# Kernel tuning notes

Measured on AMD Instinct MI355X. Metric: run time of the kernel, lower is better.

Reference implementation:

```python
import jax, jax.numpy as jnp
import numpy as np

B, S, D, H, L, V, P = 4, 1024, 768, 12, 12, 50257, 1024
HD = D // H  # 64
EPS = 1e-5


def setup_inputs() -> dict:
    key = jax.random.key(0)
    ks = jax.random.split(key, 9)
    s = 0.02
    n = lambda k, shape: (jax.random.normal(k, shape, jnp.float32) * s)
    return {
        "input_ids": jax.random.randint(ks[0], (B, S), 0, V),
        "wte": n(ks[1], (V, D)),
        "wpe": n(ks[2], (P, D)),
        "ln1_w": jnp.ones((L, D), jnp.float32),
        "ln1_b": jnp.zeros((L, D), jnp.float32),
        "attn_w": n(ks[3], (L, D, 3 * D)),
        "attn_b": jnp.zeros((L, 3 * D), jnp.float32),
        "atp_w": n(ks[4], (L, D, D)),
        "atp_b": jnp.zeros((L, D), jnp.float32),
        "ln2_w": jnp.ones((L, D), jnp.float32),
        "ln2_b": jnp.zeros((L, D), jnp.float32),
        "fc_w": n(ks[5], (L, D, 4 * D)),
        "fc_b": jnp.zeros((L, 4 * D), jnp.float32),
        "pj_w": n(ks[6], (L, 4 * D, D)),
        "pj_b": jnp.zeros((L, D), jnp.float32),
        "lnf_w": jnp.ones((D,), jnp.float32),
        "lnf_b": jnp.zeros((D,), jnp.float32),
        "lm_w": n(ks[7], (D, V)),
    }


def _ln(x, w, b):
    m = x.mean(-1, keepdims=True)
    v = ((x - m) ** 2).mean(-1, keepdims=True)
    return (x - m) * jax.lax.rsqrt(v + EPS) * w + b


def reference(input_ids, wte, wpe, ln1_w, ln1_b, attn_w, attn_b, atp_w, atp_b,
              ln2_w, ln2_b, fc_w, fc_b, pj_w, pj_b, lnf_w, lnf_b, lm_w):
    h = wte[input_ids] + wpe[jnp.arange(S)][None]  # [B,S,D]
    scale = 1.0 / jnp.sqrt(jnp.float32(HD))
    for l in range(L):
        # attention block (no causal mask in original)
        x = _ln(h, ln1_w[l], ln1_b[l])
        qkv = x @ attn_w[l] + attn_b[l]
        q, k, v = jnp.split(qkv, 3, axis=-1)
        q = q.reshape(B, S, H, HD)
        k = k.reshape(B, S, H, HD)
        v = v.reshape(B, S, H, HD)
        att = jnp.einsum('bqhd,bkhd->bhqk', q, k) * scale
        att = jax.nn.softmax(att, axis=-1)
        y = jnp.einsum('bhqk,bkhd->bqhd', att, v).reshape(B, S, D)
        h = h + y @ atp_w[l] + atp_b[l]
        # MLP block (exact erf GELU, torch nn.GELU default)
        x = _ln(h, ln2_w[l], ln2_b[l])
        h = h + jax.nn.gelu(x @ fc_w[l] + fc_b[l], approximate=False) @ pj_w[l] + pj_b[l]
    h = _ln(h, lnf_w, lnf_b)
    return h @ lm_w  # [B,S,V] logits
```

## Files before the change

### kernel.cpp

```cpp
#include <hip/hip_runtime.h>
#include <hip/hip_bf16.h>
#include <cstdint>

#define DEVI __device__ __forceinline__

typedef __attribute__((ext_vector_type(8))) short bf16x8_t;
typedef __attribute__((ext_vector_type(4))) float f32x4_t;

DEVI float bf2f(unsigned short u) {
    union { uint32_t i; float f; } v; v.i = ((uint32_t)u) << 16; return v.f;
}
DEVI unsigned short f2bf(float f) {
    union { float f; uint32_t i; } v; v.f = f;
    uint32_t i = v.i;
    uint32_t r = (i + 0x7FFFu + ((i >> 16) & 1u)) >> 16;
    return (unsigned short)r;
}

DEVI f32x4_t mfma16(bf16x8_t a, bf16x8_t b, f32x4_t c) {
    return __builtin_amdgcn_mfma_f32_16x16x32_bf16(a, b, c, 0, 0, 0);
}

#define GL2LDS(g, l) __builtin_amdgcn_global_load_lds( \
    (const __attribute__((address_space(1))) void*)(g), \
    (__attribute__((address_space(3))) void*)(l), 16, 0, 0)

__global__ void k_embed_ln(const int* __restrict__ ids, const float* __restrict__ wte,
                           const float* __restrict__ wpe, const float* __restrict__ w,
                           const float* __restrict__ b, float* __restrict__ h,
                           unsigned short* __restrict__ x) {
    int m = blockIdx.x;
    int s = m & 1023;
    int id = ids[m];
    int t = threadIdx.x;
    const float4 te = *reinterpret_cast<const float4*>(wte + (size_t)id * 768 + t * 4);
    const float4 pe = *reinterpret_cast<const float4*>(wpe + (size_t)s * 768 + t * 4);
    float4 v; v.x = te.x + pe.x; v.y = te.y + pe.y; v.z = te.z + pe.z; v.w = te.w + pe.w;
    *reinterpret_cast<float4*>(h + (size_t)m * 768 + t * 4) = v;
    float sm = v.x + v.y + v.z + v.w;
    float ss = v.x * v.x + v.y * v.y + v.z * v.z + v.w * v.w;
#pragma unroll
    for (int o = 32; o > 0; o >>= 1) { sm += __shfl_down(sm, o); ss += __shfl_down(ss, o); }
    __shared__ float red[8];
    int wid = t >> 6, lane = t & 63;
    if (lane == 0) { red[wid] = sm; red[4 + wid] = ss; }
    __syncthreads();
    if (t == 0) {
        float S = red[0] + red[1] + red[2];
        float SS = red[4] + red[5] + red[6];
        float mean = S * (1.f / 768.f);
        float var = SS * (1.f / 768.f) - mean * mean;
        red[0] = mean; red[1] = rsqrtf(var + 1e-5f);
    }
    __syncthreads();
    float mean = red[0], rst = red[1];
    float4 wv = *reinterpret_cast<const float4*>(w + t * 4);
    float4 bv = *reinterpret_cast<const float4*>(b + t * 4);
    ushort4 o4;
    o4.x = f2bf((v.x - mean) * rst * wv.x + bv.x);
    o4.y = f2bf((v.y - mean) * rst * wv.y + bv.y);
    o4.z = f2bf((v.z - mean) * rst * wv.z + bv.z);
    o4.w = f2bf((v.w - mean) * rst * wv.w + bv.w);
    *reinterpret_cast<ushort4*>(x + (size_t)m * 768 + t * 4) = o4;
}

__global__ void k_ln_red(const unsigned short* __restrict__ part, const float* __restrict__ ab,
                         const float* __restrict__ w, const float* __restrict__ b,
                         float* __restrict__ h, unsigned short* __restrict__ x) {
    int m = blockIdx.x;
    int t = threadIdx.x;
    size_t o0 = (size_t)m * 768 + t * 4;
    float4 hv = *reinterpret_cast<const float4*>(h + o0);
    ushort4 q0 = *reinterpret_cast<const ushort4*>(part + o0);
    ushort4 q1 = *reinterpret_cast<const ushort4*>(part + 4096ull * 768 + o0);
    float4 av = *reinterpret_cast<const float4*>(ab + t * 4);
    float4 v;
    v.x = hv.x + bf2f(q0.x) + bf2f(q1.x) + av.x;
    v.y = hv.y + bf2f(q0.y) + bf2f(q1.y) + av.y;
    v.z = hv.z + bf2f(q0.z) + bf2f(q1.z) + av.z;
    v.w = hv.w + bf2f(q0.w) + bf2f(q1.w) + av.w;
    float sm = v.x + v.y + v.z + v.w;
    float ss = v.x * v.x + v.y * v.y + v.z * v.z + v.w * v.w;
#pragma unroll
    for (int o = 32; o > 0; o >>= 1) { sm += __shfl_down(sm, o); ss += __shfl_down(ss, o); }
    __shared__ float red[8];
    int wid = t >> 6, lane = t & 63;
    if (lane == 0) { red[wid] = sm; red[4 + wid] = ss; }
    __syncthreads();
    if (t == 0) {
        float S = red[0] + red[1] + red[2];
        float SS = red[4] + red[5] + red[6];
        float mean = S * (1.f / 768.f);
        float var = SS * (1.f / 768.f) - mean * mean;
        red[0] = mean; red[1] = rsqrtf(var + 1e-5f);
    }
    __syncthreads();
    float mean = red[0], rst = red[1];
    *reinterpret_cast<float4*>(h + o0) = v;
    float4 wv = *reinterpret_cast<const float4*>(w + t * 4);
    float4 bv = *reinterpret_cast<const float4*>(b + t * 4);
    ushort4 o4;
    o4.x = f2bf((v.x - mean) * rst * wv.x + bv.x);
    o4.y = f2bf((v.y - mean) * rst * wv.y + bv.y);
    o4.z = f2bf((v.z - mean) * rst * wv.z + bv.z);
    o4.w = f2bf((v.w - mean) * rst * wv.w + bv.w);
    *reinterpret_cast<ushort4*>(x + (size_t)m * 768 + t * 4) = o4;
}

__global__ void k_transpose(const float* __restrict__ W, unsigned short* __restrict__ Bt,
                            int K, int N, int Npad) {
    __shared__ float tile[64][65];
    int tx = threadIdx.x, ty = threadIdx.y;
    int n0 = blockIdx.x * 64, k0 = blockIdx.y * 64;
    size_t l = blockIdx.z;
    W += l * (size_t)K * N;
    Bt += l * (size_t)Npad * K;
    if (n0 + 64 <= N) {
#pragma unroll
        for (int i = 0; i < 4; i++) {
            int kr = ty * 4 + i;
            float4 v = *reinterpret_cast<const float4*>(W + (size_t)(k0 + kr) * N + n0 + tx * 4);
            tile[kr][tx * 4 + 0] = v.x;
            tile[kr][tx * 4 + 1] = v.y;
            tile[kr][tx * 4 + 2] = v.z;
            tile[kr][tx * 4 + 3] = v.w;
        }
    } else {
#pragma unroll
        for (int i = 0; i < 4; i++) {
            int kr = ty * 4 + i;
#pragma unroll
            for (int j = 0; j < 4; j++) {
                int n = n0 + tx * 4 + j;
                tile[kr][tx * 4 + j] = (n < N) ? W[(size_t)(k0 + kr) * N + n] : 0.f;
            }
        }
    }
    __syncthreads();
#pragma unroll
    for (int i = 0; i < 4; i++) {
        int n = n0 + ty * 4 + i;
        ushort4 o;
        o.x = f2bf(tile[tx * 4 + 0][ty * 4 + i]);
        o.y = f2bf(tile[tx * 4 + 1][ty * 4 + i]);
        o.z = f2bf(tile[tx * 4 + 2][ty * 4 + i]);
        o.w = f2bf(tile[tx * 4 + 3][ty * 4 + i]);
        *reinterpret_cast<ushort4*>(Bt + (size_t)n * K + k0 + tx * 4) = o;
    }
}

template <int BM, int BIAS, int GELU, int OUTBF16, int SPLITK>
__launch_bounds__(256, 2)
__global__ void k_gemm(const unsigned short* __restrict__ A,
                       const unsigned short* __restrict__ Bt,
                       const float* __restrict__ bias,
                       void* __restrict__ out,
                       int M, int N, int K) {
    constexpr int MF = BM / 32;
    constexpr int HALF = (BM + 128) * 64;
    __shared__ char smem_raw[2 * HALF];

    int t = threadIdx.x;
    int bm = blockIdx.x, bn = blockIdx.y;
    int kc = (SPLITK > 1) ? blockIdx.z : 0;
    int KC = K / SPLITK;

    int rowA0 = bm * BM, rowB0 = bn * 128;
    int lane = t & 63, w = t >> 6;
    int wr = w >> 1, wc = w & 1;

    const unsigned short* ga0 = A  + (size_t)(rowA0 + (t >> 2)) * K + kc * KC + (t & 3) * 8;
    const unsigned short* ga1 = ga0 + (size_t)64 * K;
    const unsigned short* gb0 = Bt + (size_t)(rowB0 + (t >> 2)) * K + kc * KC + (t & 3) * 8;
    const unsigned short* gb1 = gb0 + (size_t)64 * K;

    auto stage = [&](int buf, int ktile) {
        char* dst = smem_raw + buf * HALF + t * 16;
        int kt = ktile * 32;
        GL2LDS(ga0 + kt, dst);
        if constexpr (BM == 128) GL2LDS(ga1 + kt, dst + 4096);
        char* dstB = dst + BM * 64;
        GL2LDS(gb0 + kt, dstB);
        GL2LDS(gb1 + kt, dstB + 4096);
    };

    f32x4_t acc[MF][4] = {};

    int rA = wr * (BM / 2) + (lane & 15);
    int rB = wc * 64 + (lane & 15);
    int kofs = (lane >> 4) * 8;

    const int NT = KC / 32;
    stage(0, 0);
    __syncthreads();
    int cur = 0;
    for (int kt = 0; kt < NT; kt++) {
        if (kt + 1 < NT) stage(cur ^ 1, kt + 1);
        const unsigned short* As = (const unsigned short*)(smem_raw + cur * HALF);
        const unsigned short* Bs = As + BM * 32;
        bf16x8_t a[MF], b[4];
#pragma unroll
        for (int m = 0; m < MF; m++)
            a[m] = *reinterpret_cast<const bf16x8_t*>(As + (rA + m * 16) * 32 + kofs);
#pragma unroll
        for (int n = 0; n < 4; n++)
            b[n] = *reinterpret_cast<const bf16x8_t*>(Bs + (rB + n * 16) * 32 + kofs);
#pragma unroll
        for (int m = 0; m < MF; m++)
#pragma unroll
            for (int n = 0; n < 4; n++)
                acc[m][n] = mfma16(a[m], b[n], acc[m][n]);
        __syncthreads();
        cur ^= 1;
    }

    if constexpr (OUTBF16) {
        int colBase = bn * 128 + wc * 64 + (lane & 15);
        int rowBase = bm * BM + wr * (BM / 2) + ((lane >> 4) << 2);
#pragma unroll
        for (int n = 0; n < 4; n++) {
            int col = colBase + n * 16;
            float bv = 0.f;
            if (BIAS) bv = bias[col];
#pragma unroll
            for (int m = 0; m < MF; m++) {
                int row0 = rowBase + m * 16;
#pragma unroll
                for (int r = 0; r < 4; r++) {
                    int row = row0 + r;
                    float v = acc[m][n][r] + bv;
                    if (GELU) v = 0.5f * v * (1.f + erff(v * 0.70710678118f));
                    ((unsigned short*)out)[(size_t)row * N + col] = f2bf(v);
                }
            }
        }
    } else {
        auto epi = (unsigned short (*)[16][72])smem_raw;
        unsigned short* op_base = (unsigned short*)out + (size_t)kc * M * N;
        int rowBase0 = bm * BM + wr * (BM / 2);
        int colBase0 = bn * 128 + wc * 64;
#pragma unroll
        for (int m = 0; m < MF; m++) {
#pragma unroll
            for (int n = 0; n < 4; n++)
#pragma unroll
                for (int r = 0; r < 4; r++)
                    epi[w][(lane >> 4) * 4 + r][n * 16 + (lane & 15)] = f2bf(acc[m][n][r]);
            __syncthreads();
#pragma unroll
            for (int rr = 0; rr < 4; rr++) {
                int lr = (lane >> 4) * 4 + rr;
                int grow = rowBase0 + m * 16 + lr;
                int gcol = colBase0 + (lane & 15) * 4;
                ushort4 v4 = *reinterpret_cast<ushort4*>(&epi[w][lr][(lane & 15) * 4]);
                *reinterpret_cast<ushort4*>(op_base + (size_t)grow * N + gcol) = v4;
            }
            __syncthreads();
        }
    }
}

__launch_bounds__(512, 1)
__global__ void k_lm(const unsigned short* __restrict__ A,
                     const unsigned short* __restrict__ Bt,
                     float* __restrict__ out) {
    constexpr int K = 768;
    constexpr int NT = K / 64;
    __shared__ char smem[131072];

    int t = threadIdx.x;
    int bm = blockIdx.x, bn = blockIdx.y;
    int lane = t & 63, w = t >> 6;
    int wm = w >> 2, wn = w & 3;
    int q = lane >> 4, l15 = lane & 15, l7 = lane & 7;

    int srow = t >> 3;
    int sslot = (t & 7) ^ (srow & 7);
    const unsigned short* gA = A  + (size_t)(bm * 256 + srow) * K + sslot * 8;
    const unsigned short* gB = Bt + (size_t)(bn * 256 + srow) * K + sslot * 8;

    auto stage = [&](int buf, int ktile) {
        char* dst = smem + buf * 65536 + t * 16;
        int ko = ktile * 64;
#pragma unroll
        for (int i = 0; i < 4; i++)
            GL2LDS(gA + (size_t)(i * 64) * K + ko, dst + i * 8192);
#pragma unroll
        for (int i = 0; i < 4; i++)
            GL2LDS(gB + (size_t)(i * 64) * K + ko, dst + 32768 + i * 8192);
    };

    f32x4_t acc[8][4] = {};

    stage(0, 0);
    int cur = 0;
    for (int kt = 0; kt < NT; kt++) {
        if (kt + 1 < NT) {
            stage(cur ^ 1, kt + 1);
            asm volatile("s_waitcnt vmcnt(8)" ::: "memory");
        } else {
            asm volatile("s_waitcnt vmcnt(0)" ::: "memory");
        }
        __builtin_amdgcn_s_barrier();
        asm volatile("" ::: "memory");
        const char* Ab = smem + cur * 65536;
        const char* Bb = Ab + 32768;

        bf16x8_t bfr[4][2];
#pragma unroll
        for (int nf = 0; nf < 4; nf++)
#pragma unroll
            for (int ks = 0; ks < 2; ks++) {
                int row = wn * 64 + nf * 16 + l15;
                int slot = (ks * 4 + q) ^ l7;
                bfr[nf][ks] = *reinterpret_cast<const bf16x8_t*>(Bb + row * 128 + slot * 16);
            }
#pragma unroll
        for (int p = 0; p < 4; p++) {
            bf16x8_t afr[2][2];
#pragma unroll
            for (int mi = 0; mi < 2; mi++)
#pragma unroll
                for (int ks = 0; ks < 2; ks++) {
                    int row = wm * 128 + (p * 2 + mi) * 16 + l15;
                    int slot = (ks * 4 + q) ^ l7;
                    afr[mi][ks] = *reinterpret_cast<const bf16x8_t*>(Ab + row * 128 + slot * 16);
                }
            asm volatile("s_waitcnt lgkmcnt(0)" ::: "memory");
            __builtin_amdgcn_sched_barrier(0);
            __builtin_amdgcn_s_setprio(1);
#pragma unroll
            for (int mi = 0; mi < 2; mi++)
#pragma unroll
                for (int nf = 0; nf < 4; nf++)
#pragma unroll
                    for (int ks = 0; ks < 2; ks++)
                        acc[p * 2 + mi][nf] = mfma16(afr[mi][ks], bfr[nf][ks], acc[p * 2 + mi][nf]);
            __builtin_amdgcn_s_setprio(0);
        }
        asm volatile("" ::: "memory");
        __builtin_amdgcn_s_barrier();
        cur ^= 1;
    }

    float* epi = (float*)smem + w * (16 * 68);
#pragma unroll
    for (int mf = 0; mf < 8; mf++) {
#pragma unroll
        for (int nf = 0; nf < 4; nf++)
#pragma unroll
            for (int r = 0; r < 4; r++)
                epi[(q * 4 + r) * 68 + nf * 16 + l15] = acc[mf][nf][r];
        asm volatile("s_waitcnt lgkmcnt(0)" ::: "memory");
#pragma unroll
        for (int rr = 0; rr < 4; rr++) {
            int lr = q * 4 + rr;
            int grow = bm * 256 + wm * 128 + mf * 16 + lr;
            int col0 = bn * 256 + wn * 64 + l15;
            float* op = out + (size_t)grow * 50257 + col0;
#pragma unroll
            for (int e = 0; e < 4; e++) {
                if (col0 + e * 16 < 50257) op[e * 16] = epi[lr * 68 + l15 + e * 16];
            }
        }
        asm volatile("s_waitcnt lgkmcnt(0)" ::: "memory");
    }
}

__launch_bounds__(256, 2)
__global__ void k_attn(const unsigned short* __restrict__ qkv, unsigned short* __restrict__ y) {
    __shared__ unsigned short Kb[3][4096];
    __shared__ unsigned short Vt[2][4096];
    __shared__ unsigned short Ps[4][16 * 72];

    int bh = blockIdx.y;
    int b = bh / 12, h = bh % 12;
    int qt = blockIdx.x;
    int t = threadIdx.x, lane = t & 63, w = t >> 6;
    const size_t ldq = 2304;
    const unsigned short* base = qkv + (size_t)b * 1024 * ldq + h * 64;
    const unsigned short* Kg = base + 768;

    int srow = t >> 3;
    int lslot = (t & 7) ^ (srow & 7);
    auto stageK = [&](int buf, int kt) {
#pragma unroll
        for (int i = 0; i < 2; i++) {
            const unsigned short* src = Kg + (size_t)(kt * 64 + i * 32 + srow) * ldq + lslot * 8;
            GL2LDS(src, (char*)&Kb[buf][0] + i * 4096 + t * 16);
        }
    };

    bf16x8_t qf[2];
    int qrow = qt * 64 + w * 16 + (lane & 15);
#pragma unroll
    for (int kb = 0; kb < 2; kb++)
        qf[kb] = *reinterpret_cast<const bf16x8_t*>(base + (size_t)qrow * ldq + kb * 32 + (lane >> 4) * 8);

    f32x4_t o[4] = {};
    float mrow[4], lsum[4];
#pragma unroll
    for (int r = 0; r < 4; r++) { mrow[r] = -1e30f; lsum[r] = 0.f; }
    const float scale = 0.125f;

    union VU { uint4 v[2]; unsigned short e[16]; };
    VU vv, vvn;
    {
        const unsigned short* vsrc = base + 1536 + (size_t)lane * ldq + w * 16;
        vv.v[0] = *reinterpret_cast<const uint4*>(vsrc);
        vv.v[1] = *reinterpret_cast<const uint4*>(vsrc + 8);
    }
    stageK(0, 0);
    __syncthreads();

    int cur = 0;
    for (int kt = 0; kt < 16; kt++) {
        char* vbuf = (char*)&Vt[cur][0];
#pragma unroll
        for (int j = 0; j < 16; j++) {
            int d = w * 16 + j;
            uint32_t byte = (uint32_t)(d * 128 + lane * 2) ^ (uint32_t)((d & 7) << 4);
            *(unsigned short*)(vbuf + byte) = vv.e[j];
        }
        __syncthreads();
        if (kt < 15) {
            stageK((kt + 1) % 3, kt + 1);
            const unsigned short* vsrc = base + 1536 + (size_t)((kt + 1) * 64 + lane) * ldq + w * 16;
            vvn.v[0] = *reinterpret_cast<const uint4*>(vsrc);
            vvn.v[1] = *reinterpret_cast<const uint4*>(vsrc + 8);
        }
        const char* kbuf = (const char*)&Kb[kt % 3][0];
        f32x4_t s[4] = {};
#pragma unroll
        for (int kb = 0; kb < 2; kb++) {
#pragma unroll
            for (int n = 0; n < 4; n++) {
                int row = n * 16 + (lane & 15);
                int pslot = (kb * 4 + (lane >> 4)) ^ (lane & 7);
                bf16x8_t kf = *reinterpret_cast<const bf16x8_t*>(kbuf + row * 128 + pslot * 16);
                s[n] = mfma16(qf[kb], kf, s[n]);
            }
        }
        float corr[4];
#pragma unroll
        for (int r = 0; r < 4; r++) {
            float mx = fmaxf(fmaxf(s[0][r], s[1][r]), fmaxf(s[2][r], s[3][r]));
#pragma unroll
            for (int o2 = 1; o2 < 16; o2 <<= 1) mx = fmaxf(mx, __shfl_xor(mx, o2));
            float mnew = fmaxf(mrow[r], mx * scale);
            corr[r] = __expf(mrow[r] - mnew);
            mrow[r] = mnew;
        }
        float psum[4] = {0.f, 0.f, 0.f, 0.f};
#pragma unroll
        for (int n = 0; n < 4; n++) {
#pragma unroll
            for (int r = 0; r < 4; r++) {
                float p = __expf(s[n][r] * scale - mrow[r]);
                psum[r] += p;
                int prow = (lane >> 4) * 4 + r;
                Ps[w][prow * 72 + n * 16 + (lane & 15)] = f2bf(p);
            }
        }
#pragma unroll
        for (int r = 0; r < 4; r++) {
            float ps = psum[r];
#pragma unroll
            for (int o2 = 1; o2 < 16; o2 <<= 1) ps += __shfl_xor(ps, o2);
            lsum[r] = lsum[r] * corr[r] + ps;
#pragma unroll
            for (int n = 0; n < 4; n++) o[n][r] *= corr[r];
        }
#pragma unroll
        for (int kb = 0; kb < 2; kb++) {
            bf16x8_t pf = *reinterpret_cast<const bf16x8_t*>(
                &Ps[w][(lane & 15) * 72 + kb * 32 + (lane >> 4) * 8]);
#pragma unroll
            for (int n = 0; n < 4; n++) {
                int d = n * 16 + (lane & 15);
                uint32_t byte = (uint32_t)(d * 128 + (kb * 32 + (lane >> 4) * 8) * 2)
                                ^ (uint32_t)((d & 7) << 4);
                bf16x8_t vf = *reinterpret_cast<const bf16x8_t*>(vbuf + byte);
                o[n] = mfma16(pf, vf, o[n]);
            }
        }
        vv = vvn;
        cur ^= 1;
    }
#pragma unroll
    for (int n = 0; n < 4; n++) {
#pragma unroll
        for (int r = 0; r < 4; r++) {
            float val = o[n][r] / lsum[r];
            int row = qt * 64 + w * 16 + (lane >> 4) * 4 + r;
            y[((size_t)(b * 1024 + row)) * 768 + h * 64 + n * 16 + (lane & 15)] = f2bf(val);
        }
    }
}

extern "C" void kernel_launch(void* const* d_in, const int* in_sizes, int n_in,
                              void* d_out, int out_size, void* d_ws, size_t ws_size,
                              hipStream_t stream) {
    const int*   ids   = (const int*)d_in[0];
    const float* wte   = (const float*)d_in[1];
    const float* wpe   = (const float*)d_in[2];
    const float* ln1w  = (const float*)d_in[3];
    const float* ln1b  = (const float*)d_in[4];
    const float* attnw = (const float*)d_in[5];
    const float* attnb = (const float*)d_in[6];
    const float* atpw  = (const float*)d_in[7];
    const float* atpb  = (const float*)d_in[8];
    const float* ln2w  = (const float*)d_in[9];
    const float* ln2b  = (const float*)d_in[10];
    const float* fcw   = (const float*)d_in[11];
    const float* fcb   = (const float*)d_in[12];
    const float* pjw   = (const float*)d_in[13];
    const float* pjb   = (const float*)d_in[14];
    const float* lnfw  = (const float*)d_in[15];
    const float* lnfb  = (const float*)d_in[16];
    const float* lmw   = (const float*)d_in[17];
    float* out = (float*)d_out;

    char* ws = (char*)d_ws;
    size_t off = 0;
    auto alloc = [&](size_t bytes) -> void* {
        void* p = ws + off;
        off += (bytes + 255) & ~(size_t)255;
        return p;
    };
    float*          h      = (float*)alloc(4096ull * 768 * 4);
    unsigned short* x      = (unsigned short*)alloc(4096ull * 768 * 2);
    unsigned short* qkvb   = (unsigned short*)alloc(4096ull * 2304 * 2);
    unsigned short* y      = (unsigned short*)alloc(4096ull * 768 * 2);
    unsigned short* u      = (unsigned short*)alloc(4096ull * 3072 * 2);
    unsigned short* part   = (unsigned short*)alloc(2ull * 4096 * 768 * 2);
    unsigned short* attnwT = (unsigned short*)alloc(12ull * 2304 * 768 * 2);
    unsigned short* atpwT  = (unsigned short*)alloc(12ull * 768 * 768 * 2);
    unsigned short* fcwT   = (unsigned short*)alloc(12ull * 3072 * 768 * 2);
    unsigned short* pjwT   = (unsigned short*)alloc(12ull * 768 * 3072 * 2);
    unsigned short* lmwT   = (unsigned short*)alloc(50432ull * 768 * 2);

    dim3 tb(16, 16);
    k_transpose<<<dim3(2304 / 64, 768 / 64, 12), tb, 0, stream>>>(attnw, attnwT, 768, 2304, 2304);
    k_transpose<<<dim3(768 / 64, 768 / 64, 12), tb, 0, stream>>>(atpw, atpwT, 768, 768, 768);
    k_transpose<<<dim3(3072 / 64, 768 / 64, 12), tb, 0, stream>>>(fcw, fcwT, 768, 3072, 3072);
    k_transpose<<<dim3(768 / 64, 3072 / 64, 12), tb, 0, stream>>>(pjw, pjwT, 3072, 768, 768);
    k_transpose<<<dim3(50432 / 64, 768 / 64, 1), tb, 0, stream>>>(lmw, lmwT, 768, 50257, 50432);

    k_embed_ln<<<4096, 192, 0, stream>>>(ids, wte, wpe, ln1w, ln1b, h, x);

    for (int l = 0; l < 12; l++) {
        k_gemm<128, 1, 0, 1, 1><<<dim3(32, 18), 256, 0, stream>>>(
            x, attnwT + (size_t)l * 2304 * 768, attnb + l * 2304, qkvb,
            4096, 2304, 768);
        k_attn<<<dim3(16, 48), 256, 0, stream>>>(qkvb, y);
        k_gemm<64, 0, 0, 0, 2><<<dim3(64, 6, 2), 256, 0, stream>>>(
            y, atpwT + (size_t)l * 768 * 768, nullptr, part,
            4096, 768, 768);
        k_ln_red<<<4096, 192, 0, stream>>>(part, atpb + l * 768,
            ln2w + l * 768, ln2b + l * 768, h, x);
        k_gemm<128, 1, 1, 1, 1><<<dim3(32, 24), 256, 0, stream>>>(
            x, fcwT + (size_t)l * 3072 * 768, fcb + l * 3072, u,
            4096, 3072, 768);
        k_gemm<64, 0, 0, 0, 2><<<dim3(64, 6, 2), 256, 0, stream>>>(
            u, pjwT + (size_t)l * 768 * 3072, nullptr, part,
            4096, 768, 3072);
        const float* nw = (l < 11) ? ln1w + (l + 1) * 768 : lnfw;
        const float* nb = (l < 11) ? ln1b + (l + 1) * 768 : lnfb;
        k_ln_red<<<4096, 192, 0, stream>>>(part, pjb + l * 768, nw, nb, h, x);
    }
    k_lm<<<dim3(16, 197), 512, 0, stream>>>(x, lmwT, out);
}
```

Measured before the change: 2.801 ms.

## Transpose QK^T MFMA so each lane owns a query row; lazy softmax rescale

Swaps the MFMA operands in the attention kernel so each lane holds scores for a single query row. Row max and sum then need only two cross-lane shuffles instead of a 16-lane butterfly per row. It also adds a threshold-based lazy rescale that updates the running max and rescales the output only when some row's max grows by more than 8. This cuts shuffle and exp work in the softmax inner loop, at the cost of extra shuffles to redistribute correction factors and a small numeric-range risk from the deferred max update.

```diff
diff --git a/kernel.cpp b/kernel.cpp
--- a/kernel.cpp
+++ b/kernel.cpp
@@ -398,9 +398,7 @@
         qf[kb] = *reinterpret_cast<const bf16x8_t*>(base + (size_t)qrow * ldq + kb * 32 + (lane >> 4) * 8);
 
     f32x4_t o[4] = {};
-    float mrow[4], lsum[4];
-#pragma unroll
-    for (int r = 0; r < 4; r++) { mrow[r] = -1e30f; lsum[r] = 0.f; }
+    float m = -1e30f, l = 0.f;
     const float scale = 0.125f;
 
     union VU { uint4 v[2]; unsigned short e[16]; };
@@ -438,39 +436,41 @@
                 int row = n * 16 + (lane & 15);
                 int pslot = (kb * 4 + (lane >> 4)) ^ (lane & 7);
                 bf16x8_t kf = *reinterpret_cast<const bf16x8_t*>(kbuf + row * 128 + pslot * 16);
-                s[n] = mfma16(qf[kb], kf, s[n]);
-            }
-        }
-        float corr[4];
-#pragma unroll
-        for (int r = 0; r < 4; r++) {
-            float mx = fmaxf(fmaxf(s[0][r], s[1][r]), fmaxf(s[2][r], s[3][r]));
-#pragma unroll
-            for (int o2 = 1; o2 < 16; o2 <<= 1) mx = fmaxf(mx, __shfl_xor(mx, o2));
-            float mnew = fmaxf(mrow[r], mx * scale);
-            corr[r] = __expf(mrow[r] - mnew);
-            mrow[r] = mnew;
-        }
-        float psum[4] = {0.f, 0.f, 0.f, 0.f};
-#pragma unroll
-        for (int n = 0; n < 4; n++) {
+                s[n] = mfma16(kf, qf[kb], s[n]);
+            }
+        }
+        float tmax = s[0][0];
+#pragma unroll
+        for (int n = 0; n < 4; n++)
+#pragma unroll
+            for (int r = 0; r < 4; r++) tmax = fmaxf(tmax, s[n][r]);
+        tmax = fmaxf(tmax, __shfl_xor(tmax, 16));
+        tmax = fmaxf(tmax, __shfl_xor(tmax, 32));
+        tmax *= scale;
+        if (__any(tmax > m + 8.f)) {
+            float mnew = fmaxf(m, tmax);
+            float corr = __expf(m - mnew);
+            m = mnew;
+            l *= corr;
 #pragma unroll
             for (int r = 0; r < 4; r++) {
-                float p = __expf(s[n][r] * scale - mrow[r]);
-                psum[r] += p;
-                int prow = (lane >> 4) * 4 + r;
-                Ps[w][prow * 72 + n * 16 + (lane & 15)] = f2bf(p);
-            }
-        }
-#pragma unroll
-        for (int r = 0; r < 4; r++) {
-            float ps = psum[r];
-#pragma unroll
-            for (int o2 = 1; o2 < 16; o2 <<= 1) ps += __shfl_xor(ps, o2);
-            lsum[r] = lsum[r] * corr[r] + ps;
-#pragma unroll
-            for (int n = 0; n < 4; n++) o[n][r] *= corr[r];
-        }
+                float cr = __shfl(corr, (lane & 48) | ((lane >> 4) * 4 + r));
+#pragma unroll
+                for (int n = 0; n < 4; n++) o[n][r] *= cr;
+            }
+        }
+        float psum = 0.f;
+#pragma unroll
+        for (int n = 0; n < 4; n++)
+#pragma unroll
+            for (int r = 0; r < 4; r++) {
+                float p = __expf(s[n][r] * scale - m);
+                psum += p;
+                Ps[w][(lane & 15) * 72 + n * 16 + (lane >> 4) * 4 + r] = f2bf(p);
+            }
+        psum += __shfl_xor(psum, 16);
+        psum += __shfl_xor(psum, 32);
+        l += psum;
 #pragma unroll
         for (int kb = 0; kb < 2; kb++) {
             bf16x8_t pf = *reinterpret_cast<const bf16x8_t*>(
@@ -487,11 +487,15 @@
         vv = vvn;
         cur ^= 1;
     }
+    float linv[4];
+#pragma unroll
+    for (int r = 0; r < 4; r++)
+        linv[r] = 1.f / __shfl(l, (lane & 48) | ((lane >> 4) * 4 + r));
 #pragma unroll
     for (int n = 0; n < 4; n++) {
 #pragma unroll
         for (int r = 0; r < 4; r++) {
-            float val = o[n][r] / lsum[r];
+            float val = o[n][r] * linv[r];
             int row = qt * 64 + w * 16 + (lane >> 4) * 4 + r;
             y[((size_t)(b * 1024 + row)) * 768 + h * 64 + n * 16 + (lane & 15)] = f2bf(val);
         }
```

Measured after the change: 2.623 ms. 1.07x faster.
